# Kernel optimization log

Measured on AMD Instinct MI355X. Metric: run time of the kernel, lower is better.

## Reference

```python
import jax, jax.numpy as jnp
import numpy as np

N = 20000   # nodes
E = 320000  # directed edges (before self-loops)
D = 64      # input_dim
H = 10      # GAT heads
HD = H * D  # 640
NEG_SLOPE = 0.2


def setup_inputs() -> dict:
    key = jax.random.key(0)
    ks = jax.random.split(key, 10)
    return {
        "x": jax.random.normal(ks[0], (N, D), jnp.float32),
        "W_gat": jax.random.normal(ks[1], (D, HD), jnp.float32) / np.sqrt(D).astype(np.float32),
        "att_src": jax.random.normal(ks[2], (H, D), jnp.float32) / np.sqrt(D).astype(np.float32),
        "att_dst": jax.random.normal(ks[3], (H, D), jnp.float32) / np.sqrt(D).astype(np.float32),
        "b_gat": jnp.zeros((HD,), jnp.float32),
        "W_gcn": jax.random.normal(ks[4], (HD, HD), jnp.float32) / np.sqrt(HD).astype(np.float32),
        "b_gcn": jnp.zeros((HD,), jnp.float32),
        "W1": jax.random.normal(ks[5], (2 * HD, 1500), jnp.float32) / np.sqrt(2 * HD).astype(np.float32),
        "b1": jnp.zeros((1500,), jnp.float32),
        "W2": jax.random.normal(ks[6], (1500, 10), jnp.float32) / np.sqrt(1500).astype(np.float32),
        "b2": jnp.zeros((10,), jnp.float32),
        "edge_index": jax.random.randint(ks[7], (2, E), 0, N, dtype=jnp.int64),
    }


def _forward(x, W_gat, att_src, att_dst, b_gat, W_gcn, b_gcn, W1, b1, W2, b2, edge_index):
    n = x.shape[0]
    # add self-loops (PyG default for both GATConv and GCNConv)
    loop = jnp.arange(n, dtype=edge_index.dtype)
    ei = jnp.concatenate([edge_index, jnp.stack([loop, loop])], axis=1)
    src, dst = ei[0], ei[1]

    # ---- GATConv(D -> D, heads=H, concat) ----
    xl = (x @ W_gat).reshape(n, H, D)                      # [N,H,D]
    a_src = jnp.einsum('nhd,hd->nh', xl, att_src)          # [N,H]
    a_dst = jnp.einsum('nhd,hd->nh', xl, att_dst)          # [N,H]
    alpha = jax.nn.leaky_relu(a_src[src] + a_dst[dst], NEG_SLOPE)  # [E',H]
    m = jax.ops.segment_max(alpha, dst, num_segments=n)    # segment softmax over incoming edges
    ex = jnp.exp(alpha - m[dst])
    den = jax.ops.segment_sum(ex, dst, num_segments=n)
    w = ex / (den[dst] + 1e-16)                            # [E',H]
    msg = xl[src] * w[:, :, None]                          # [E',H,D]
    x1 = jax.ops.segment_sum(msg, dst, num_segments=n).reshape(n, HD) + b_gat
    x1 = jax.nn.relu(x1)

    # ---- GCNConv(HD -> HD), symmetric norm with self-loops ----
    deg = jax.ops.segment_sum(jnp.ones(ei.shape[1], x.dtype), dst, num_segments=n)
    dinv = jnp.where(deg > 0, jax.lax.rsqrt(deg), 0.0)
    norm = dinv[src] * dinv[dst]                           # [E']
    xw = x1 @ W_gcn                                        # [N,HD]
    x2 = jax.ops.segment_sum(xw[src] * norm[:, None], dst, num_segments=n) + b_gcn
    x2 = jax.nn.relu(x2)

    # ---- global max/mean pool (batch=None -> single graph) + MLP head ----
    pooled = jnp.concatenate([x2.max(axis=0, keepdims=True),
                              x2.mean(axis=0, keepdims=True)], axis=1)  # [1, 2*HD]
    h = jax.nn.relu(pooled @ W1 + b1)
    # dropout is identity in eval mode
    return h @ W2 + b2                                     # [1, 10]


def reference(x, W_gat, att_src, att_dst, b_gat, W_gcn, b_gcn, W1, b1, W2, b2, edge_index):
    return _forward(x, W_gat, att_src, att_dst, b_gat, W_gcn, b_gcn, W1, b1, W2, b2, edge_index)
```

## Files before the change

### kernel.cpp

```cpp
#include <hip/hip_runtime.h>
#include <hip/hip_bf16.h>
#include <math.h>

#define NN 20000
#define DD 64
#define HH 10
#define HDIM 640
#define NEG 0.2f
#define H1 1500
#define ASTRIDE 12
#define BKK 128

typedef _Float16 half8 __attribute__((ext_vector_type(8)));
typedef _Float16 half4v __attribute__((ext_vector_type(4)));
typedef _Float16 half2v __attribute__((ext_vector_type(2)));
typedef float f32x4 __attribute__((ext_vector_type(4)));

__global__ __launch_bounds__(256) void k_cvtB(const float* __restrict__ Wgcn,
                                              const float* __restrict__ Wg,
                                              _Float16* __restrict__ Wbt,
                                              _Float16* __restrict__ WgT)
{
    __shared__ float t[32][33];
    const int bx = blockIdx.x;
    int by = blockIdx.y;
    const float* W; _Float16* WT; int rows, cols;
    if (by < 20) { W = Wgcn; WT = Wbt; rows = HDIM; cols = HDIM; }
    else         { W = Wg;   WT = WgT; rows = DD;   cols = HDIM; by -= 20; }
    const int lx = threadIdx.x & 31, ly = threadIdx.x >> 5;
    #pragma unroll
    for (int i = ly; i < 32; i += 8)
        t[i][lx] = W[(size_t)(by * 32 + i) * cols + bx * 32 + lx];
    __syncthreads();
    #pragma unroll
    for (int j = ly; j < 32; j += 8)
        WT[(size_t)(bx * 32 + j) * rows + by * 32 + lx] = (_Float16)t[lx][j];
}

__global__ __launch_bounds__(256) void k_gemm1(
    const float* __restrict__ x, const _Float16* __restrict__ WgT,
    const float* __restrict__ att_s, const float* __restrict__ att_d,
    _Float16* __restrict__ xl, float* __restrict__ a_src, float* __restrict__ a_dst)
{
    __shared__ _Float16 As[128][72];
    __shared__ _Float16 Bs[64][72];
    const int tid = threadIdx.x;
    const int m0 = blockIdx.x * 128;
    const int h  = blockIdx.y;
    const int n0 = h * 64;

    {
        const int row = tid >> 1, ch = (tid & 1) * 32;
        const int gr = m0 + row;
        if (gr < NN) {
            const float* xp = &x[(size_t)gr * DD + ch];
            #pragma unroll
            for (int i = 0; i < 8; ++i) {
                const float4 v = *(const float4*)&xp[i * 4];
                half4v o = {(_Float16)v.x, (_Float16)v.y, (_Float16)v.z, (_Float16)v.w};
                *(half4v*)&As[row][ch + i * 4] = o;
            }
        } else {
            const half8 z = {0, 0, 0, 0, 0, 0, 0, 0};
            #pragma unroll
            for (int i = 0; i < 4; ++i) *(half8*)&As[row][ch + i * 8] = z;
        }
    }
    {
        const int row = tid >> 2, part = (tid & 3) * 16;
        const _Float16* wp = &WgT[(size_t)(n0 + row) * DD + part];
        *(half8*)&Bs[row][part]     = *(const half8*)&wp[0];
        *(half8*)&Bs[row][part + 8] = *(const half8*)&wp[8];
    }
    __syncthreads();

    const int lane = tid & 63, wave = tid >> 6;
    const int l15 = lane & 15, quad = lane >> 4;
    f32x4 acc[2][4];
    #pragma unroll
    for (int r = 0; r < 2; ++r)
        #pragma unroll
        for (int c = 0; c < 4; ++c) acc[r][c] = (f32x4){0.f, 0.f, 0.f, 0.f};

    #pragma unroll
    for (int ks = 0; ks < 2; ++ks) {
        const half8 a0 = *(const half8*)&As[wave * 32 + l15][ks * 32 + quad * 8];
        const half8 a1 = *(const half8*)&As[wave * 32 + 16 + l15][ks * 32 + quad * 8];
        #pragma unroll
        for (int c = 0; c < 4; ++c) {
            const half8 b = *(const half8*)&Bs[c * 16 + l15][ks * 32 + quad * 8];
            acc[0][c] = __builtin_amdgcn_mfma_f32_16x16x32_f16(a0, b, acc[0][c], 0, 0, 0);
            acc[1][c] = __builtin_amdgcn_mfma_f32_16x16x32_f16(a1, b, acc[1][c], 0, 0, 0);
        }
    }

    float asv[4], adv[4];
    #pragma unroll
    for (int c = 0; c < 4; ++c) {
        asv[c] = att_s[h * DD + c * 16 + l15];
        adv[c] = att_d[h * DD + c * 16 + l15];
    }
    #pragma unroll
    for (int r = 0; r < 2; ++r) {
        float ps[4] = {0.f, 0.f, 0.f, 0.f}, pd[4] = {0.f, 0.f, 0.f, 0.f};
        #pragma unroll
        for (int c = 0; c < 4; ++c)
            #pragma unroll
            for (int g = 0; g < 4; ++g) {
                ps[g] = fmaf(acc[r][c][g], asv[c], ps[g]);
                pd[g] = fmaf(acc[r][c][g], adv[c], pd[g]);
            }
        #pragma unroll
        for (int m = 1; m <= 8; m <<= 1)
            #pragma unroll
            for (int g = 0; g < 4; ++g) {
                ps[g] += __shfl_xor(ps[g], m);
                pd[g] += __shfl_xor(pd[g], m);
            }
        #pragma unroll
        for (int c = 0; c < 4; ++c)
            #pragma unroll
            for (int g = 0; g < 4; ++g) {
                const int row = m0 + wave * 32 + r * 16 + quad * 4 + g;
                if (row < NN)
                    xl[(size_t)row * HDIM + n0 + c * 16 + l15] = (_Float16)acc[r][c][g];
            }
        if (l15 == 0)
            #pragma unroll
            for (int g = 0; g < 4; ++g) {
                const int row = m0 + wave * 32 + r * 16 + quad * 4 + g;
                if (row < NN) {
                    a_src[(size_t)row * ASTRIDE + h] = ps[g];
                    a_dst[(size_t)row * ASTRIDE + h] = pd[g];
                }
            }
    }
}

__global__ void k_count(const int* __restrict__ ei, int E, int* __restrict__ cnt)
{
    const int e = blockIdx.x * blockDim.x + threadIdx.x;
    if (e >= E + NN) return;
    const int d = (e < E) ? ei[E + e] : (e - E);
    atomicAdd(&cnt[d], 1);
}

__global__ __launch_bounds__(1024) void k_scan(const int* __restrict__ cnt,
                                               int* __restrict__ rowptr,
                                               float* __restrict__ dinv)
{
    __shared__ int sh[1024];
    const int t = threadIdx.x;
    const int CH = 20;
    const int base = t * CH;
    int loc[CH];
    int s = 0;
    #pragma unroll
    for (int i = 0; i < CH; ++i) {
        const int idx = base + i;
        const int c = (idx < NN) ? cnt[idx] : 0;
        loc[i] = s; s += c;
    }
    sh[t] = s; __syncthreads();
    for (int off = 1; off < 1024; off <<= 1) {
        const int v = (t >= off) ? sh[t - off] : 0;
        __syncthreads();
        sh[t] += v;
        __syncthreads();
    }
    const int prev = (t == 0) ? 0 : sh[t - 1];
    #pragma unroll
    for (int i = 0; i < CH; ++i) {
        const int idx = base + i;
        if (idx < NN) {
            rowptr[idx] = prev + loc[i];
            dinv[idx]   = rsqrtf((float)cnt[idx]);
        }
    }
    if (t == 1023) rowptr[NN] = sh[1023];
}

__global__ void k_fill(const int* __restrict__ ei, int E,
                       const int* __restrict__ rowptr,
                       int* __restrict__ cursor, int* __restrict__ csr,
                       const float* __restrict__ dinv, float* __restrict__ wn,
                       const float* __restrict__ aS, const float* __restrict__ aD,
                       float* __restrict__ wgat)
{
    const int e = blockIdx.x * blockDim.x + threadIdx.x;
    if (e >= E + NN) return;
    int s, d;
    if (e < E) { s = ei[e]; d = ei[E + e]; } else { s = d = e - E; }
    const int pos = atomicAdd(&cursor[d], 1);
    const int idx = rowptr[d] + pos;
    csr[idx] = s;
    wn[idx]  = dinv[s] * dinv[d];

    const f32x4 s0 = *(const f32x4*)&aS[(size_t)s * ASTRIDE];
    const f32x4 s1 = *(const f32x4*)&aS[(size_t)s * ASTRIDE + 4];
    const float2 s2 = *(const float2*)&aS[(size_t)s * ASTRIDE + 8];
    const f32x4 d0 = *(const f32x4*)&aD[(size_t)d * ASTRIDE];
    const f32x4 d1 = *(const f32x4*)&aD[(size_t)d * ASTRIDE + 4];
    const float2 d2 = *(const float2*)&aD[(size_t)d * ASTRIDE + 8];
    const float av[10] = {s0.x + d0.x, s0.y + d0.y, s0.z + d0.z, s0.w + d0.w,
                          s1.x + d1.x, s1.y + d1.y, s1.z + d1.z, s1.w + d1.w,
                          s2.x + d2.x, s2.y + d2.y};
    float* wp = &wgat[(size_t)idx * HH];
    #pragma unroll
    for (int h = 0; h < 10; ++h) {
        float a = av[h];
        a = (a >= 0.f) ? a : NEG * a;
        wp[h] = __expf(a);
    }
}

__global__ __launch_bounds__(256) void k_gat_gather(
    const int* __restrict__ rowptr, const int* __restrict__ csr,
    const float* __restrict__ wgat, const _Float16* __restrict__ xl,
    const float* __restrict__ b_gat, _Float16* __restrict__ x1)
{
    const int wave = threadIdx.x >> 6, lane = threadIdx.x & 63;
    const int n = blockIdx.x * 4 + wave;
    const int c0 = lane * 8;
    const int h0 = lane >> 3;
    const bool dual = (lane < 16);
    const int c1 = 512 + lane * 8;
    const int h1 = 8 + (lane >> 3);

    float acc0[8], acc1[8], ws0 = 0.f, ws1 = 0.f;
    #pragma unroll
    for (int i = 0; i < 8; ++i) { acc0[i] = 0.f; acc1[i] = 0.f; }

    const int j0 = rowptr[n], j1 = rowptr[n + 1];
    int j = j0;
    for (; j + 3 < j1; j += 4) {
        const int sA = csr[j], sB = csr[j + 1], sC = csr[j + 2], sD = csr[j + 3];
        const float wA0 = wgat[(size_t)(j + 0) * HH + h0];
        const float wB0 = wgat[(size_t)(j + 1) * HH + h0];
        const float wC0 = wgat[(size_t)(j + 2) * HH + h0];
        const float wD0 = wgat[(size_t)(j + 3) * HH + h0];
        ws0 += wA0 + wB0 + wC0 + wD0;
        const half8 vA0 = *(const half8*)&xl[(size_t)sA * HDIM + c0];
        const half8 vB0 = *(const half8*)&xl[(size_t)sB * HDIM + c0];
        const half8 vC0 = *(const half8*)&xl[(size_t)sC * HDIM + c0];
        const half8 vD0 = *(const half8*)&xl[(size_t)sD * HDIM + c0];
        #pragma unroll
        for (int i = 0; i < 8; ++i) {
            acc0[i] = fmaf(wA0, (float)vA0[i], acc0[i]);
            acc0[i] = fmaf(wB0, (float)vB0[i], acc0[i]);
            acc0[i] = fmaf(wC0, (float)vC0[i], acc0[i]);
            acc0[i] = fmaf(wD0, (float)vD0[i], acc0[i]);
        }
        if (dual) {
            const float wA1 = wgat[(size_t)(j + 0) * HH + h1];
            const float wB1 = wgat[(size_t)(j + 1) * HH + h1];
            const float wC1 = wgat[(size_t)(j + 2) * HH + h1];
            const float wD1 = wgat[(size_t)(j + 3) * HH + h1];
            ws1 += wA1 + wB1 + wC1 + wD1;
            const half8 vA1 = *(const half8*)&xl[(size_t)sA * HDIM + c1];
            const half8 vB1 = *(const half8*)&xl[(size_t)sB * HDIM + c1];
            const half8 vC1 = *(const half8*)&xl[(size_t)sC * HDIM + c1];
            const half8 vD1 = *(const half8*)&xl[(size_t)sD * HDIM + c1];
            #pragma unroll
            for (int i = 0; i < 8; ++i) {
                acc1[i] = fmaf(wA1, (float)vA1[i], acc1[i]);
                acc1[i] = fmaf(wB1, (float)vB1[i], acc1[i]);
                acc1[i] = fmaf(wC1, (float)vC1[i], acc1[i]);
                acc1[i] = fmaf(wD1, (float)vD1[i], acc1[i]);
            }
        }
    }
    for (; j < j1; ++j) {
        const int sA = csr[j];
        const float wA0 = wgat[(size_t)j * HH + h0];
        ws0 += wA0;
        const half8 vA0 = *(const half8*)&xl[(size_t)sA * HDIM + c0];
        #pragma unroll
        for (int i = 0; i < 8; ++i) acc0[i] = fmaf(wA0, (float)vA0[i], acc0[i]);
        if (dual) {
            const float wA1 = wgat[(size_t)j * HH + h1];
            ws1 += wA1;
            const half8 vA1 = *(const half8*)&xl[(size_t)sA * HDIM + c1];
            #pragma unroll
            for (int i = 0; i < 8; ++i) acc1[i] = fmaf(wA1, (float)vA1[i], acc1[i]);
        }
    }

    {
        const float rr = 1.f / (ws0 + 1e-16f);
        const float4 ba = *(const float4*)&b_gat[c0];
        const float4 bb = *(const float4*)&b_gat[c0 + 4];
        const float bv[8] = {ba.x, ba.y, ba.z, ba.w, bb.x, bb.y, bb.z, bb.w};
        half8 o;
        #pragma unroll
        for (int i = 0; i < 8; ++i) {
            const float v = fmaf(acc0[i], rr, bv[i]);
            o[i] = (_Float16)((v > 0.f) ? v : 0.f);
        }
        *(half8*)&x1[(size_t)n * HDIM + c0] = o;
    }
    if (dual) {
        const float rr = 1.f / (ws1 + 1e-16f);
        const float4 ba = *(const float4*)&b_gat[c1];
        const float4 bb = *(const float4*)&b_gat[c1 + 4];
        const float bv[8] = {ba.x, ba.y, ba.z, ba.w, bb.x, bb.y, bb.z, bb.w};
        half8 o;
        #pragma unroll
        for (int i = 0; i < 8; ++i) {
            const float v = fmaf(acc1[i], rr, bv[i]);
            o[i] = (_Float16)((v > 0.f) ? v : 0.f);
        }
        *(half8*)&x1[(size_t)n * HDIM + c1] = o;
    }
}

__global__ __launch_bounds__(256) void k_gcn_gather(
    const int* __restrict__ rowptr, const int* __restrict__ csr,
    const float* __restrict__ wn, const _Float16* __restrict__ x1,
    _Float16* __restrict__ t)
{
    const int wave = threadIdx.x >> 6, lane = threadIdx.x & 63;
    const int n = blockIdx.x * 4 + wave;
    const int c0 = lane * 8;
    const bool dual = (lane < 16);
    const int c1 = 512 + lane * 8;

    float acc0[8], acc1[8];
    #pragma unroll
    for (int i = 0; i < 8; ++i) { acc0[i] = 0.f; acc1[i] = 0.f; }

    const int j0 = rowptr[n], j1 = rowptr[n + 1];
    int j = j0;
    for (; j + 3 < j1; j += 4) {
        const int sA = csr[j], sB = csr[j + 1], sC = csr[j + 2], sD = csr[j + 3];
        const float wA = wn[j], wB = wn[j + 1], wC = wn[j + 2], wD = wn[j + 3];
        const half8 vA0 = *(const half8*)&x1[(size_t)sA * HDIM + c0];
        const half8 vB0 = *(const half8*)&x1[(size_t)sB * HDIM + c0];
        const half8 vC0 = *(const half8*)&x1[(size_t)sC * HDIM + c0];
        const half8 vD0 = *(const half8*)&x1[(size_t)sD * HDIM + c0];
        #pragma unroll
        for (int i = 0; i < 8; ++i) {
            acc0[i] = fmaf(wA, (float)vA0[i], acc0[i]);
            acc0[i] = fmaf(wB, (float)vB0[i], acc0[i]);
            acc0[i] = fmaf(wC, (float)vC0[i], acc0[i]);
            acc0[i] = fmaf(wD, (float)vD0[i], acc0[i]);
        }
        if (dual) {
            const half8 vA1 = *(const half8*)&x1[(size_t)sA * HDIM + c1];
            const half8 vB1 = *(const half8*)&x1[(size_t)sB * HDIM + c1];
            const half8 vC1 = *(const half8*)&x1[(size_t)sC * HDIM + c1];
            const half8 vD1 = *(const half8*)&x1[(size_t)sD * HDIM + c1];
            #pragma unroll
            for (int i = 0; i < 8; ++i) {
                acc1[i] = fmaf(wA, (float)vA1[i], acc1[i]);
                acc1[i] = fmaf(wB, (float)vB1[i], acc1[i]);
                acc1[i] = fmaf(wC, (float)vC1[i], acc1[i]);
                acc1[i] = fmaf(wD, (float)vD1[i], acc1[i]);
            }
        }
    }
    for (; j < j1; ++j) {
        const int sA = csr[j];
        const float wA = wn[j];
        const half8 vA0 = *(const half8*)&x1[(size_t)sA * HDIM + c0];
        #pragma unroll
        for (int i = 0; i < 8; ++i) acc0[i] = fmaf(wA, (float)vA0[i], acc0[i]);
        if (dual) {
            const half8 vA1 = *(const half8*)&x1[(size_t)sA * HDIM + c1];
            #pragma unroll
            for (int i = 0; i < 8; ++i) acc1[i] = fmaf(wA, (float)vA1[i], acc1[i]);
        }
    }

    {
        half8 o;
        #pragma unroll
        for (int i = 0; i < 8; ++i) o[i] = (_Float16)acc0[i];
        *(half8*)&t[(size_t)n * HDIM + c0] = o;
    }
    if (dual) {
        half8 o;
        #pragma unroll
        for (int i = 0; i < 8; ++i) o[i] = (_Float16)acc1[i];
        *(half8*)&t[(size_t)n * HDIM + c1] = o;
    }
}

__global__ __launch_bounds__(256) void k_gemm2(const _Float16* __restrict__ X,
                                               const _Float16* __restrict__ Wbt,
                                               const float* __restrict__ b_gcn,
                                               float* __restrict__ pmax,
                                               float* __restrict__ psum)
{
    __shared__ _Float16 Bs[128 * BKK];
    const int tid = threadIdx.x;
    const int lane = tid & 63, wave = tid >> 6;
    const int l15 = lane & 15, quad = lane >> 4;
    const int m0 = blockIdx.x * 128 + wave * 32;
    const int n0 = blockIdx.y * 128;
    const int l7 = l15 & 7;

    f32x4 acc[2][8];
    #pragma unroll
    for (int r = 0; r < 2; ++r)
        #pragma unroll
        for (int c = 0; c < 8; ++c) acc[r][c] = (f32x4){0.f, 0.f, 0.f, 0.f};

    const int jrow = lane >> 4;
    const int jchunk = lane & 15;

    const _Float16* a0p = &X[(size_t)(m0 + l15) * HDIM + quad * 8];
    const _Float16* a1p = a0p + (size_t)16 * HDIM;

    for (int kb = 0; kb < HDIM; kb += BKK) {
        #pragma unroll
        for (int i = 0; i < 8; ++i) {
            const int r = (wave * 8 + i) * 4 + jrow;
            const int ck = jchunk ^ (r & 7);
            const _Float16* src = &Wbt[(size_t)(n0 + r) * HDIM + kb + ck * 8];
            __builtin_amdgcn_global_load_lds(
                (const __attribute__((address_space(1))) void*)src,
                (__attribute__((address_space(3))) void*)&Bs[(size_t)(wave * 8 + i) * 512],
                16, 0, 0);
        }
        half8 a0[4], a1[4];
        #pragma unroll
        for (int ks = 0; ks < 4; ++ks) {
            a0[ks] = *(const half8*)(a0p + kb + ks * 32);
            a1[ks] = *(const half8*)(a1p + kb + ks * 32);
        }
        __syncthreads();
        #pragma unroll
        for (int ks = 0; ks < 4; ++ks) {
            #pragma unroll
            for (int c = 0; c < 8; ++c) {
                const int br = c * 16 + l15;
                const int ck = (4 * ks + quad) ^ l7;
                const half8 b = *(const half8*)&Bs[(size_t)br * BKK + ck * 8];
                acc[0][c] = __builtin_amdgcn_mfma_f32_16x16x32_f16(a0[ks], b, acc[0][c], 0, 0, 0);
                acc[1][c] = __builtin_amdgcn_mfma_f32_16x16x32_f16(a1[ks], b, acc[1][c], 0, 0, 0);
            }
        }
        __syncthreads();
    }

    float lmax[8], lsum[8];
    #pragma unroll
    for (int c = 0; c < 8; ++c) { lmax[c] = 0.f; lsum[c] = 0.f; }
    #pragma unroll
    for (int c = 0; c < 8; ++c) {
        const float bb = b_gcn[n0 + c * 16 + l15];
        #pragma unroll
        for (int r = 0; r < 2; ++r)
            #pragma unroll
            for (int g = 0; g < 4; ++g) {
                const int row = m0 + r * 16 + quad * 4 + g;
                if (row < NN) {
                    float v = acc[r][c][g] + bb;
                    v = (v > 0.f) ? v : 0.f;
                    lmax[c] = fmaxf(lmax[c], v);
                    lsum[c] += v;
                }
            }
    }
    float* redm = (float*)Bs;
    float* reds = redm + 128;
    if (tid < 128) { redm[tid] = 0.f; reds[tid] = 0.f; }
    __syncthreads();
    #pragma unroll
    for (int c = 0; c < 8; ++c) {
        const int col = c * 16 + l15;
        atomicMax((int*)&redm[col], __float_as_int(lmax[c]));
        atomicAdd(&reds[col], lsum[c]);
    }
    __syncthreads();
    if (tid < 128) {
        atomicMax((int*)&pmax[n0 + tid], __float_as_int(redm[tid]));
        atomicAdd(&psum[n0 + tid], reds[tid]);
    }
}

__global__ __launch_bounds__(256) void k_mlp1(const float* __restrict__ pmax,
                                              const float* __restrict__ psum,
                                              const float* __restrict__ W1,
                                              float* __restrict__ hacc)
{
    __shared__ float pl[80];
    const int t = threadIdx.x;
    const int i0 = blockIdx.y * 80;
    if (t < 80) {
        const int i = i0 + t;
        pl[t] = (i < HDIM) ? pmax[i] : psum[i - HDIM] * (1.0f / NN);
    }
    __syncthreads();
    const int j = blockIdx.x * 256 + t;
    if (j >= H1) return;
    float acc = 0.f;
    #pragma unroll 8
    for (int i = 0; i < 80; ++i)
        acc = fmaf(pl[i], W1[(size_t)(i0 + i) * H1 + j], acc);
    atomicAdd(&hacc[j], acc);
}

__global__ __launch_bounds__(256) void k_mlp2(const float* __restrict__ hacc,
                                              const float* __restrict__ b1,
                                              const float* __restrict__ W2,
                                              const float* __restrict__ b2,
                                              float* __restrict__ out)
{
    __shared__ float hsh[H1];
    __shared__ float red[256];
    const int t = threadIdx.x;
    for (int i = t; i < H1; i += 256) {
        const float v = hacc[i] + b1[i];
        hsh[i] = (v > 0.f) ? v : 0.f;
    }
    __syncthreads();
    float acc[10];
    #pragma unroll
    for (int k = 0; k < 10; ++k) acc[k] = 0.f;
    for (int i = t; i < H1; i += 256) {
        const float h = hsh[i];
        #pragma unroll
        for (int k = 0; k < 10; ++k) acc[k] = fmaf(h, W2[i * 10 + k], acc[k]);
    }
    for (int k = 0; k < 10; ++k) {
        red[t] = acc[k]; __syncthreads();
        for (int s2 = 128; s2 > 0; s2 >>= 1) {
            if (t < s2) red[t] += red[t + s2];
            __syncthreads();
        }
        if (t == 0) out[k] = red[0] + b2[k];
        __syncthreads();
    }
}

extern "C" void kernel_launch(void* const* d_in, const int* in_sizes, int n_in,
                              void* d_out, int out_size, void* d_ws, size_t ws_size,
                              hipStream_t stream)
{
    const float* x     = (const float*)d_in[0];
    const float* Wg    = (const float*)d_in[1];
    const float* att_s = (const float*)d_in[2];
    const float* att_d = (const float*)d_in[3];
    const float* b_gat = (const float*)d_in[4];
    const float* Wgcn  = (const float*)d_in[5];
    const float* b_gcn = (const float*)d_in[6];
    const float* W1    = (const float*)d_in[7];
    const float* b1    = (const float*)d_in[8];
    const float* W2    = (const float*)d_in[9];
    const float* b2    = (const float*)d_in[10];
    const int*   ei    = (const int*)d_in[11];
    const int E = in_sizes[11] / 2;
    const int EP = E + NN;
    float* out = (float*)d_out;

    char* wsp = (char*)d_ws;
    size_t off = 0;
    auto alc = [&](size_t b) { void* p = wsp + off; off += (b + 255) & ~(size_t)255; return p; };
    _Float16* bufA = (_Float16*)alc((size_t)NN * HDIM * 2);
    _Float16* bufB = (_Float16*)alc((size_t)NN * HDIM * 2);
    float* aS     = (float*)alc((size_t)NN * ASTRIDE * 4);
    float* aD     = (float*)alc((size_t)NN * ASTRIDE * 4);
    int*   rowptr = (int*)alc((size_t)(NN + 1) * 4);
    int*   csr    = (int*)alc((size_t)EP * 4);
    float* dinv   = (float*)alc((size_t)NN * 4);
    float* wn     = (float*)alc((size_t)EP * 4);
    float* wgat   = (float*)alc((size_t)EP * HH * 4);
    _Float16* Wbt = (_Float16*)alc((size_t)HDIM * HDIM * 2);
    _Float16* WgT = (_Float16*)alc((size_t)HDIM * DD * 2);
    const size_t zoff = off;
    int*   cnt    = (int*)alc((size_t)NN * 4);
    int*   cursor = (int*)alc((size_t)NN * 4);
    float* pmax   = (float*)alc((size_t)HDIM * 4);
    float* psum   = (float*)alc((size_t)HDIM * 4);
    float* hacc   = (float*)alc((size_t)H1 * 4);
    const size_t zsize = off - zoff;

    hipMemsetAsync(cnt, 0, zsize, stream);

    dim3 gw(HDIM / 32, HDIM / 32 + DD / 32);
    k_cvtB<<<gw, 256, 0, stream>>>(Wgcn, Wg, Wbt, WgT);
    dim3 g1((NN + 127) / 128, HH);
    k_gemm1<<<g1, 256, 0, stream>>>(x, WgT, att_s, att_d, bufA, aS, aD);
    k_count<<<(EP + 255) / 256, 256, 0, stream>>>(ei, E, cnt);
    k_scan<<<1, 1024, 0, stream>>>(cnt, rowptr, dinv);
    k_fill<<<(EP + 255) / 256, 256, 0, stream>>>(ei, E, rowptr, cursor, csr,
                                                 dinv, wn, aS, aD, wgat);
    k_gat_gather<<<NN / 4, 256, 0, stream>>>(rowptr, csr, wgat, bufA, b_gat, bufB);
    k_gcn_gather<<<NN / 4, 256, 0, stream>>>(rowptr, csr, wn, bufB, bufA);
    dim3 g2((NN + 127) / 128, HDIM / 128);
    k_gemm2<<<g2, 256, 0, stream>>>(bufA, Wbt, b_gcn, pmax, psum);
    dim3 gm1(6, 16);
    k_mlp1<<<gm1, 256, 0, stream>>>(pmax, psum, W1, hacc);
    k_mlp2<<<1, 256, 0, stream>>>(hacc, b1, W2, b2, out);
}
```

Baseline: 366.4 us.

## Split gather kernels by 64-column slice with edge-parallel lanes and XCD-aware block mapping

Both neighbour-gather kernels now assign one wave per (node, 64-column slice) instead of one wave per whole 640-wide node row. The eight 8-lane groups in a wave each walk every eighth edge and are combined with a shuffle reduction. This removes the idle lanes of the old dual-pass layout and exposes more memory-level parallelism. GAT attention weights are stored head-major so each slice reads a contiguous weight stream. A block-index mapping (bid&7) places blocks of the same column slice on the same XCD, which is meant to improve L2 locality of the gathered feature columns. In exchange there are ten times more blocks, repeated rowptr/csr reads per slice, and shuffle-reduction overhead.

```diff
diff --git a/kernel.cpp b/kernel.cpp
--- a/kernel.cpp
+++ b/kernel.cpp
@@ -10,10 +10,10 @@
 #define H1 1500
 #define ASTRIDE 12
 #define BKK 128
+#define NB 5000
 
 typedef _Float16 half8 __attribute__((ext_vector_type(8)));
 typedef _Float16 half4v __attribute__((ext_vector_type(4)));
-typedef _Float16 half2v __attribute__((ext_vector_type(2)));
 typedef float f32x4 __attribute__((ext_vector_type(4)));
 
 __global__ __launch_bounds__(256) void k_cvtB(const float* __restrict__ Wgcn,
@@ -185,10 +185,11 @@
                        int* __restrict__ cursor, int* __restrict__ csr,
                        const float* __restrict__ dinv, float* __restrict__ wn,
                        const float* __restrict__ aS, const float* __restrict__ aD,
-                       float* __restrict__ wgat)
-{
+                       float* __restrict__ wgatT)
+{
+    const int EP = E + NN;
     const int e = blockIdx.x * blockDim.x + threadIdx.x;
-    if (e >= E + NN) return;
+    if (e >= EP) return;
     int s, d;
     if (e < E) { s = ei[e]; d = ei[E + e]; } else { s = d = e - E; }
     const int pos = atomicAdd(&cursor[d], 1);
@@ -205,184 +206,115 @@
     const float av[10] = {s0.x + d0.x, s0.y + d0.y, s0.z + d0.z, s0.w + d0.w,
                           s1.x + d1.x, s1.y + d1.y, s1.z + d1.z, s1.w + d1.w,
                           s2.x + d2.x, s2.y + d2.y};
-    float* wp = &wgat[(size_t)idx * HH];
     #pragma unroll
     for (int h = 0; h < 10; ++h) {
         float a = av[h];
         a = (a >= 0.f) ? a : NEG * a;
-        wp[h] = __expf(a);
-    }
-}
-
-__global__ __launch_bounds__(256) void k_gat_gather(
+        wgatT[(size_t)h * EP + idx] = __expf(a);
+    }
+}
+
+__device__ __forceinline__ void slice_map(int bid, int& s, int& m)
+{
+    const int r = bid & 7, k = bid >> 3;
+    if (k < NB) { s = r; m = k; }
+    else        { s = 8 + (r & 1); m = ((r >> 1) * 1250) + (k - NB); }
+}
+
+__global__ __launch_bounds__(256) void k_gat_gather2(
     const int* __restrict__ rowptr, const int* __restrict__ csr,
-    const float* __restrict__ wgat, const _Float16* __restrict__ xl,
-    const float* __restrict__ b_gat, _Float16* __restrict__ x1)
-{
-    const int wave = threadIdx.x >> 6, lane = threadIdx.x & 63;
-    const int n = blockIdx.x * 4 + wave;
-    const int c0 = lane * 8;
-    const int h0 = lane >> 3;
-    const bool dual = (lane < 16);
-    const int c1 = 512 + lane * 8;
-    const int h1 = 8 + (lane >> 3);
-
-    float acc0[8], acc1[8], ws0 = 0.f, ws1 = 0.f;
-    #pragma unroll
-    for (int i = 0; i < 8; ++i) { acc0[i] = 0.f; acc1[i] = 0.f; }
-
-    const int j0 = rowptr[n], j1 = rowptr[n + 1];
-    int j = j0;
-    for (; j + 3 < j1; j += 4) {
-        const int sA = csr[j], sB = csr[j + 1], sC = csr[j + 2], sD = csr[j + 3];
-        const float wA0 = wgat[(size_t)(j + 0) * HH + h0];
-        const float wB0 = wgat[(size_t)(j + 1) * HH + h0];
-        const float wC0 = wgat[(size_t)(j + 2) * HH + h0];
-        const float wD0 = wgat[(size_t)(j + 3) * HH + h0];
-        ws0 += wA0 + wB0 + wC0 + wD0;
-        const half8 vA0 = *(const half8*)&xl[(size_t)sA * HDIM + c0];
-        const half8 vB0 = *(const half8*)&xl[(size_t)sB * HDIM + c0];
-        const half8 vC0 = *(const half8*)&xl[(size_t)sC * HDIM + c0];
-        const half8 vD0 = *(const half8*)&xl[(size_t)sD * HDIM + c0];
-        #pragma unroll
-        for (int i = 0; i < 8; ++i) {
-            acc0[i] = fmaf(wA0, (float)vA0[i], acc0[i]);
-            acc0[i] = fmaf(wB0, (float)vB0[i], acc0[i]);
-            acc0[i] = fmaf(wC0, (float)vC0[i], acc0[i]);
-            acc0[i] = fmaf(wD0, (float)vD0[i], acc0[i]);
-        }
-        if (dual) {
-            const float wA1 = wgat[(size_t)(j + 0) * HH + h1];
-            const float wB1 = wgat[(size_t)(j + 1) * HH + h1];
-            const float wC1 = wgat[(size_t)(j + 2) * HH + h1];
-            const float wD1 = wgat[(size_t)(j + 3) * HH + h1];
-            ws1 += wA1 + wB1 + wC1 + wD1;
-            const half8 vA1 = *(const half8*)&xl[(size_t)sA * HDIM + c1];
-            const half8 vB1 = *(const half8*)&xl[(size_t)sB * HDIM + c1];
-            const half8 vC1 = *(const half8*)&xl[(size_t)sC * HDIM + c1];
-            const half8 vD1 = *(const half8*)&xl[(size_t)sD * HDIM + c1];
-            #pragma unroll
-            for (int i = 0; i < 8; ++i) {
-                acc1[i] = fmaf(wA1, (float)vA1[i], acc1[i]);
-                acc1[i] = fmaf(wB1, (float)vB1[i], acc1[i]);
-                acc1[i] = fmaf(wC1, (float)vC1[i], acc1[i]);
-                acc1[i] = fmaf(wD1, (float)vD1[i], acc1[i]);
-            }
-        }
-    }
-    for (; j < j1; ++j) {
-        const int sA = csr[j];
-        const float wA0 = wgat[(size_t)j * HH + h0];
-        ws0 += wA0;
-        const half8 vA0 = *(const half8*)&xl[(size_t)sA * HDIM + c0];
-        #pragma unroll
-        for (int i = 0; i < 8; ++i) acc0[i] = fmaf(wA0, (float)vA0[i], acc0[i]);
-        if (dual) {
-            const float wA1 = wgat[(size_t)j * HH + h1];
-            ws1 += wA1;
-            const half8 vA1 = *(const half8*)&xl[(size_t)sA * HDIM + c1];
-            #pragma unroll
-            for (int i = 0; i < 8; ++i) acc1[i] = fmaf(wA1, (float)vA1[i], acc1[i]);
-        }
-    }
-
-    {
-        const float rr = 1.f / (ws0 + 1e-16f);
-        const float4 ba = *(const float4*)&b_gat[c0];
-        const float4 bb = *(const float4*)&b_gat[c0 + 4];
+    const float* __restrict__ wgatT, const _Float16* __restrict__ xl,
+    const float* __restrict__ b_gat, _Float16* __restrict__ x1, int EP)
+{
+    int s, m;
+    slice_map(blockIdx.x, s, m);
+    const int n = m * 4 + (threadIdx.x >> 6);
+    const int lane = threadIdx.x & 63;
+    const int g = lane >> 3, l = lane & 7;
+    const int col = s * 64 + l * 8;
+    const float* __restrict__ wp = wgatT + (size_t)s * EP;
+
+    float acc[8];
+    #pragma unroll
+    for (int i = 0; i < 8; ++i) acc[i] = 0.f;
+    float ws = 0.f;
+
+    const int j1 = rowptr[n + 1];
+    int j = rowptr[n] + g;
+    int src0 = 0; float w0 = 0.f;
+    if (j < j1) { src0 = csr[j]; w0 = wp[j]; }
+    while (j < j1) {
+        const int jn = j + 8;
+        int src1 = 0; float w1 = 0.f;
+        if (jn < j1) { src1 = csr[jn]; w1 = wp[jn]; }
+        const half8 v = *(const half8*)&xl[(size_t)src0 * HDIM + col];
+        ws += w0;
+        #pragma unroll
+        for (int i = 0; i < 8; ++i) acc[i] = fmaf(w0, (float)v[i], acc[i]);
+        j = jn; src0 = src1; w0 = w1;
+    }
+
+    #pragma unroll
+    for (int mk = 8; mk <= 32; mk <<= 1) {
+        ws += __shfl_xor(ws, mk);
+        #pragma unroll
+        for (int i = 0; i < 8; ++i) acc[i] += __shfl_xor(acc[i], mk);
+    }
+    if (g == 0) {
+        const float rr = 1.f / (ws + 1e-16f);
+        const float4 ba = *(const float4*)&b_gat[col];
+        const float4 bb = *(const float4*)&b_gat[col + 4];
         const float bv[8] = {ba.x, ba.y, ba.z, ba.w, bb.x, bb.y, bb.z, bb.w};
         half8 o;
         #pragma unroll
         for (int i = 0; i < 8; ++i) {
-            const float v = fmaf(acc0[i], rr, bv[i]);
-            o[i] = (_Float16)((v > 0.f) ? v : 0.f);
-        }
-        *(half8*)&x1[(size_t)n * HDIM + c0] = o;
-    }
-    if (dual) {
-        const float rr = 1.f / (ws1 + 1e-16f);
-        const float4 ba = *(const float4*)&b_gat[c1];
-        const float4 bb = *(const float4*)&b_gat[c1 + 4];
-        const float bv[8] = {ba.x, ba.y, ba.z, ba.w, bb.x, bb.y, bb.z, bb.w};
-        half8 o;
-        #pragma unroll
-        for (int i = 0; i < 8; ++i) {
-            const float v = fmaf(acc1[i], rr, bv[i]);
-            o[i] = (_Float16)((v > 0.f) ? v : 0.f);
-        }
-        *(half8*)&x1[(size_t)n * HDIM + c1] = o;
-    }
-}
-
-__global__ __launch_bounds__(256) void k_gcn_gather(
+            const float v2 = fmaf(acc[i], rr, bv[i]);
+            o[i] = (_Float16)((v2 > 0.f) ? v2 : 0.f);
+        }
+        *(half8*)&x1[(size_t)n * HDIM + col] = o;
+    }
+}
+
+__global__ __launch_bounds__(256) void k_gcn_gather2(
     const int* __restrict__ rowptr, const int* __restrict__ csr,
     const float* __restrict__ wn, const _Float16* __restrict__ x1,
     _Float16* __restrict__ t)
 {
-    const int wave = threadIdx.x >> 6, lane = threadIdx.x & 63;
-    const int n = blockIdx.x * 4 + wave;
-    const int c0 = lane * 8;
-    const bool dual = (lane < 16);
-    const int c1 = 512 + lane * 8;
-
-    float acc0[8], acc1[8];
-    #pragma unroll
-    for (int i = 0; i < 8; ++i) { acc0[i] = 0.f; acc1[i] = 0.f; }
-
-    const int j0 = rowptr[n], j1 = rowptr[n + 1];
-    int j = j0;
-    for (; j + 3 < j1; j += 4) {
-        const int sA = csr[j], sB = csr[j + 1], sC = csr[j + 2], sD = csr[j + 3];
-        const float wA = wn[j], wB = wn[j + 1], wC = wn[j + 2], wD = wn[j + 3];
-        const half8 vA0 = *(const half8*)&x1[(size_t)sA * HDIM + c0];
-        const half8 vB0 = *(const half8*)&x1[(size_t)sB * HDIM + c0];
-        const half8 vC0 = *(const half8*)&x1[(size_t)sC * HDIM + c0];
-        const half8 vD0 = *(const half8*)&x1[(size_t)sD * HDIM + c0];
-        #pragma unroll
-        for (int i = 0; i < 8; ++i) {
-            acc0[i] = fmaf(wA, (float)vA0[i], acc0[i]);
-            acc0[i] = fmaf(wB, (float)vB0[i], acc0[i]);
-            acc0[i] = fmaf(wC, (float)vC0[i], acc0[i]);
-            acc0[i] = fmaf(wD, (float)vD0[i], acc0[i]);
-        }
-        if (dual) {
-            const half8 vA1 = *(const half8*)&x1[(size_t)sA * HDIM + c1];
-            const half8 vB1 = *(const half8*)&x1[(size_t)sB * HDIM + c1];
-            const half8 vC1 = *(const half8*)&x1[(size_t)sC * HDIM + c1];
-            const half8 vD1 = *(const half8*)&x1[(size_t)sD * HDIM + c1];
-            #pragma unroll
-            for (int i = 0; i < 8; ++i) {
-                acc1[i] = fmaf(wA, (float)vA1[i], acc1[i]);
-                acc1[i] = fmaf(wB, (float)vB1[i], acc1[i]);
-                acc1[i] = fmaf(wC, (float)vC1[i], acc1[i]);
-                acc1[i] = fmaf(wD, (float)vD1[i], acc1[i]);
-            }
-        }
-    }
-    for (; j < j1; ++j) {
-        const int sA = csr[j];
-        const float wA = wn[j];
-        const half8 vA0 = *(const half8*)&x1[(size_t)sA * HDIM + c0];
-        #pragma unroll
-        for (int i = 0; i < 8; ++i) acc0[i] = fmaf(wA, (float)vA0[i], acc0[i]);
-        if (dual) {
-            const half8 vA1 = *(const half8*)&x1[(size_t)sA * HDIM + c1];
-            #pragma unroll
-            for (int i = 0; i < 8; ++i) acc1[i] = fmaf(wA, (float)vA1[i], acc1[i]);
-        }
-    }
-
-    {
+    int s, m;
+    slice_map(blockIdx.x, s, m);
+    const int n = m * 4 + (threadIdx.x >> 6);
+    const int lane = threadIdx.x & 63;
+    const int g = lane >> 3, l = lane & 7;
+    const int col = s * 64 + l * 8;
+
+    float acc[8];
+    #pragma unroll
+    for (int i = 0; i < 8; ++i) acc[i] = 0.f;
+
+    const int j1 = rowptr[n + 1];
+    int j = rowptr[n] + g;
+    int src0 = 0; float w0 = 0.f;
+    if (j < j1) { src0 = csr[j]; w0 = wn[j]; }
+    while (j < j1) {
+        const int jn = j + 8;
+        int src1 = 0; float w1 = 0.f;
+        if (jn < j1) { src1 = csr[jn]; w1 = wn[jn]; }
+        const half8 v = *(const half8*)&x1[(size_t)src0 * HDIM + col];
+        #pragma unroll
+        for (int i = 0; i < 8; ++i) acc[i] = fmaf(w0, (float)v[i], acc[i]);
+        j = jn; src0 = src1; w0 = w1;
+    }
+
+    #pragma unroll
+    for (int mk = 8; mk <= 32; mk <<= 1) {
+        #pragma unroll
+        for (int i = 0; i < 8; ++i) acc[i] += __shfl_xor(acc[i], mk);
+    }
+    if (g == 0) {
         half8 o;
         #pragma unroll
-        for (int i = 0; i < 8; ++i) o[i] = (_Float16)acc0[i];
-        *(half8*)&t[(size_t)n * HDIM + c0] = o;
-    }
-    if (dual) {
-        half8 o;
-        #pragma unroll
-        for (int i = 0; i < 8; ++i) o[i] = (_Float16)acc1[i];
-        *(half8*)&t[(size_t)n * HDIM + c1] = o;
+        for (int i = 0; i < 8; ++i) o[i] = (_Float16)acc[i];
+        *(half8*)&t[(size_t)n * HDIM + col] = o;
     }
 }
 
@@ -566,7 +498,7 @@
     int*   csr    = (int*)alc((size_t)EP * 4);
     float* dinv   = (float*)alc((size_t)NN * 4);
     float* wn     = (float*)alc((size_t)EP * 4);
-    float* wgat   = (float*)alc((size_t)EP * HH * 4);
+    float* wgatT  = (float*)alc((size_t)EP * HH * 4);
     _Float16* Wbt = (_Float16*)alc((size_t)HDIM * HDIM * 2);
     _Float16* WgT = (_Float16*)alc((size_t)HDIM * DD * 2);
     const size_t zoff = off;
@@ -586,9 +518,9 @@
     k_count<<<(EP + 255) / 256, 256, 0, stream>>>(ei, E, cnt);
     k_scan<<<1, 1024, 0, stream>>>(cnt, rowptr, dinv);
     k_fill<<<(EP + 255) / 256, 256, 0, stream>>>(ei, E, rowptr, cursor, csr,
-                                                 dinv, wn, aS, aD, wgat);
-    k_gat_gather<<<NN / 4, 256, 0, stream>>>(rowptr, csr, wgat, bufA, b_gat, bufB);
-    k_gcn_gather<<<NN / 4, 256, 0, stream>>>(rowptr, csr, wn, bufB, bufA);
+                                                 dinv, wn, aS, aD, wgatT);
+    k_gat_gather2<<<NB * 10, 256, 0, stream>>>(rowptr, csr, wgatT, bufA, b_gat, bufB, EP);
+    k_gcn_gather2<<<NB * 10, 256, 0, stream>>>(rowptr, csr, wn, bufB, bufA);
     dim3 g2((NN + 127) / 128, HDIM / 128);
     k_gemm2<<<g2, 256, 0, stream>>>(bufA, Wbt, b_gcn, pmax, psum);
     dim3 gm1(6, 16);
```

New measurement: 424.6 us. +15.9%, slower.
